# Optimization experiments

Hardware: AMD Instinct MI355X
Metric: run time of the kernel (lower is better)

## Reference

```python
import jax, jax.numpy as jnp
import numpy as np

E, H, D, F = 768, 12, 64, 3072
SCALE = D ** -0.5
EPS = 1e-5


def setup_inputs() -> dict:
    key = jax.random.key(0)
    ks = jax.random.split(key, 12)
    B, S = 8, 1024
    x = jax.random.normal(ks[0], (B, S, E), jnp.float32)
    # causal additive mask: 0 on/below diagonal, large negative above
    causal = jnp.triu(jnp.full((S, S), -1e9, jnp.float32), k=1)
    mask = jnp.broadcast_to(causal, (B, 1, S, S))
    init = lambda k, shp: jax.random.normal(k, shp, jnp.float32) * (shp[0] ** -0.5)
    return {
        "x": x, "mask": mask,
        "ln1_g": jnp.ones((E,), jnp.float32), "ln1_b": jnp.zeros((E,), jnp.float32),
        "wq": init(ks[1], (E, E)), "bq": jnp.zeros((E,), jnp.float32),
        "wk": init(ks[2], (E, E)), "bk": jnp.zeros((E,), jnp.float32),
        "wv": init(ks[3], (E, E)), "bv": jnp.zeros((E,), jnp.float32),
        "wo": init(ks[4], (E, E)), "bo": jnp.zeros((E,), jnp.float32),
        "ln2_g": jnp.ones((E,), jnp.float32), "ln2_b": jnp.zeros((E,), jnp.float32),
        "w1": init(ks[5], (E, F)), "b1": jnp.zeros((F,), jnp.float32),
        "w2": init(ks[6], (F, E)), "b2": jnp.zeros((E,), jnp.float32),
    }


def _layernorm(x, g, b):
    mu = jnp.mean(x, axis=-1, keepdims=True)
    var = jnp.var(x, axis=-1, keepdims=True)
    return (x - mu) * jax.lax.rsqrt(var + EPS) * g + b


def _attention(h, mask, wq, bq, wk, bk, wv, bv, wo, bo):
    B, S, _ = h.shape
    split = lambda t: t.reshape(B, S, H, D).transpose(0, 2, 1, 3)  # (B,H,S,D)
    q = split((h @ wq + bq) * SCALE)
    k = split(h @ wk + bk)
    v = split(h @ wv + bv)
    scores = jnp.einsum("bhqd,bhkd->bhqk", q, k) + mask
    attn = jax.nn.softmax(scores, axis=-1)
    o = jnp.einsum("bhqk,bhkd->bhqd", attn, v)
    o = o.transpose(0, 2, 1, 3).reshape(B, S, E)
    return o @ wo + bo


def reference(x, mask, ln1_g, ln1_b, wq, bq, wk, bk, wv, bv, wo, bo,
              ln2_g, ln2_b, w1, b1, w2, b2):
    h = _layernorm(x, ln1_g, ln1_b)
    h = x + _attention(h, mask, wq, bq, wk, bk, wv, bv, wo, bo)
    m = _layernorm(h, ln2_g, ln2_b)
    m = jax.nn.gelu(m @ w1 + b1, approximate=False) @ w2 + b2
    return h + m
```

## Files before the change

### kernel.cpp

```cpp
#include <hip/hip_runtime.h>
#include <hip/hip_bf16.h>

#define E_ 768
#define H_ 12
#define D_ 64
#define F_ 3072
#define S_ 1024
#define B_ 8
#define R_ 8192

typedef __attribute__((ext_vector_type(4))) float f32x4;
typedef __attribute__((ext_vector_type(8))) short bf16x8;

__device__ __forceinline__ short f2bf(float f) {
  unsigned u = __builtin_bit_cast(unsigned, f);
  u = (u + 0x7FFFu + ((u >> 16) & 1u)) >> 16;
  return (short)u;
}

__device__ __forceinline__ f32x4 mfma16(bf16x8 a, bf16x8 b, f32x4 c) {
  return __builtin_amdgcn_mfma_f32_16x16x32_bf16(a, b, c, 0, 0, 0);
}

#define GLD_LDS(g, l) __builtin_amdgcn_global_load_lds( \
    (const __attribute__((address_space(1))) void*)(g), \
    (__attribute__((address_space(3))) void*)(l), 16, 0, 0)

__global__ __launch_bounds__(256) void transpose_cast_kernel(
    const float* __restrict__ src, short* __restrict__ dst, int K, int N, float scale) {
  __shared__ float t[32][33];
  int k0 = blockIdx.x * 32, n0 = blockIdx.y * 32;
  int tr = threadIdx.x >> 5, tc = threadIdx.x & 31;
#pragma unroll
  for (int i = 0; i < 4; i++) {
    int r = i * 8 + tr;
    t[r][tc] = src[(long)(k0 + r) * N + n0 + tc] * scale;
  }
  __syncthreads();
#pragma unroll
  for (int i = 0; i < 4; i++) {
    int r = i * 8 + tr;
    dst[(long)(n0 + r) * K + k0 + tc] = f2bf(t[tc][r]);
  }
}

__global__ __launch_bounds__(256) void biasprep_kernel(
    const float* __restrict__ bq, const float* __restrict__ bk,
    const float* __restrict__ bv, float* __restrict__ dst) {
  int i = blockIdx.x * 256 + threadIdx.x;
  const float QS = 0.125f * 1.44269504088896340736f;
  if (i < 2304) {
    dst[i] = i < 768 ? QS * bq[i] : (i < 1536 ? bk[i - 768] : bv[i - 1536]);
  }
}

__global__ __launch_bounds__(256) void ln_kernel(
    const float* __restrict__ in, const float* __restrict__ g,
    const float* __restrict__ bb, short* __restrict__ outp) {
  int w = threadIdx.x >> 6, l = threadIdx.x & 63;
  long row = (long)blockIdx.x * 4 + w;
  const float4* r4 = (const float4*)(in + row * E_);
  float4 v[3];
  float s = 0.f, ss = 0.f;
#pragma unroll
  for (int i = 0; i < 3; i++) {
    v[i] = r4[i * 64 + l];
    s += v[i].x + v[i].y + v[i].z + v[i].w;
    ss += v[i].x * v[i].x + v[i].y * v[i].y + v[i].z * v[i].z + v[i].w * v[i].w;
  }
#pragma unroll
  for (int m = 1; m < 64; m <<= 1) { s += __shfl_xor(s, m); ss += __shfl_xor(ss, m); }
  float mu = s * (1.f / E_);
  float inv = rsqrtf(ss * (1.f / E_) - mu * mu + 1e-5f);
  const float4* g4 = (const float4*)g;
  const float4* b4 = (const float4*)bb;
  short4* o4 = (short4*)(outp + row * E_);
#pragma unroll
  for (int i = 0; i < 3; i++) {
    float4 gg = g4[i * 64 + l], bv = b4[i * 64 + l];
    short4 o;
    o.x = f2bf((v[i].x - mu) * inv * gg.x + bv.x);
    o.y = f2bf((v[i].y - mu) * inv * gg.y + bv.y);
    o.z = f2bf((v[i].z - mu) * inv * gg.z + bv.z);
    o.w = f2bf((v[i].w - mu) * inv * gg.w + bv.w);
    o4[i * 64 + l] = o;
  }
}

__global__ __launch_bounds__(256) void transpose_v_kernel(
    const short* __restrict__ v, short* __restrict__ vt) {
  __shared__ short t[64][68];
  int sb = blockIdx.x, p = blockIdx.y;
  const short* src = v + ((long)p * S_ + sb * 64) * 64;
  int tid = threadIdx.x;
#pragma unroll
  for (int i = 0; i < 4; i++) {
    int lin = tid + i * 256;
    int s = lin >> 4, c4 = lin & 15;
    short4 val = *(const short4*)(src + s * 64 + c4 * 4);
    t[s][c4 * 4 + 0] = val.x; t[s][c4 * 4 + 1] = val.y;
    t[s][c4 * 4 + 2] = val.z; t[s][c4 * 4 + 3] = val.w;
  }
  __syncthreads();
#pragma unroll
  for (int i = 0; i < 4; i++) {
    int lin = tid + i * 256;
    int d = lin >> 4, c4 = lin & 15;
    short4 o;
    o.x = t[c4 * 4 + 0][d]; o.y = t[c4 * 4 + 1][d];
    o.z = t[c4 * 4 + 2][d]; o.w = t[c4 * 4 + 3][d];
    *(short4*)(vt + ((long)p * 64 + d) * S_ + sb * 64 + c4 * 4) = o;
  }
}

template <int EPI>
__global__ __launch_bounds__(256) void gemm_bt(
    const short* __restrict__ A, const short* __restrict__ BT,
    const float* __restrict__ bias, const float* __restrict__ res,
    void* __restrict__ o0, void* __restrict__ o1, void* __restrict__ o2,
    int M, int N, int K) {
  __shared__ short lA[128 * 32];
  __shared__ short lB[128 * 32];
  int tid = threadIdx.x;
  int bm = blockIdx.x, bn = blockIdx.y;
  int w = tid >> 6, l = tid & 63;
  int wr = w >> 1, wc = w & 1;
  int lr = l & 15, lg = l >> 4;

  const f32x4 fz = {0.f, 0.f, 0.f, 0.f};
  f32x4 acc[4][4];
#pragma unroll
  for (int i = 0; i < 4; i++)
#pragma unroll
    for (int j = 0; j < 4; j++) acc[i][j] = fz;

  const short* Ab = A + (long)bm * 128 * K;
  const short* Bb = BT + (long)bn * 128 * K;
  int r0 = tid >> 2, kk0 = (tid & 3) * 8;
  int wb = (tid & 192) * 8;

  for (int k0 = 0; k0 < K; k0 += 32) {
    const short* ga0 = Ab + (long)r0 * K + k0 + kk0;
    const short* gb0 = Bb + (long)r0 * K + k0 + kk0;
    GLD_LDS(ga0, lA + wb);
    GLD_LDS(ga0 + (long)64 * K, lA + 2048 + wb);
    GLD_LDS(gb0, lB + wb);
    GLD_LDS(gb0 + (long)64 * K, lB + 2048 + wb);
    __syncthreads();
    bf16x8 af[4], bf[4];
#pragma unroll
    for (int m = 0; m < 4; m++) af[m] = *(const bf16x8*)&lA[(wr * 64 + m * 16 + lr) * 32 + lg * 8];
#pragma unroll
    for (int n = 0; n < 4; n++) bf[n] = *(const bf16x8*)&lB[(wc * 64 + n * 16 + lr) * 32 + lg * 8];
#pragma unroll
    for (int m = 0; m < 4; m++)
#pragma unroll
      for (int n = 0; n < 4; n++) acc[m][n] = mfma16(af[m], bf[n], acc[m][n]);
    __syncthreads();
  }

  int rb = bm * 128 + wr * 64;
  int cb = bn * 128 + wc * 64;
  if constexpr (EPI == 0) {
    int part = (bn * 128) / 768;
    short* dst = part == 0 ? (short*)o0 : (part == 1 ? (short*)o1 : (short*)o2);
#pragma unroll
    for (int m = 0; m < 4; m++)
#pragma unroll
      for (int n = 0; n < 4; n++) {
        int col = cb + n * 16 + lr;
        int e = col - part * 768;
        int hh = e >> 6, d = e & 63;
        float bc = bias[col];
#pragma unroll
        for (int r = 0; r < 4; r++) {
          int row = rb + m * 16 + lg * 4 + r;
          int bbi = row >> 10, sI = row & 1023;
          dst[((long)(bbi * H_ + hh) * S_ + sI) * D_ + d] = f2bf(acc[m][n][r] + bc);
        }
      }
  } else if constexpr (EPI == 1) {
    float* o = (float*)o0;
#pragma unroll
    for (int m = 0; m < 4; m++)
#pragma unroll
      for (int n = 0; n < 4; n++) {
        int col = cb + n * 16 + lr;
        float bc = bias[col];
#pragma unroll
        for (int r = 0; r < 4; r++) {
          long idx = (long)(rb + m * 16 + lg * 4 + r) * N + col;
          o[idx] = acc[m][n][r] + bc + res[idx];
        }
      }
  } else {
    short* o = (short*)o0;
#pragma unroll
    for (int m = 0; m < 4; m++)
#pragma unroll
      for (int n = 0; n < 4; n++) {
        int col = cb + n * 16 + lr;
        float bc = bias[col];
#pragma unroll
        for (int r = 0; r < 4; r++) {
          long idx = (long)(rb + m * 16 + lg * 4 + r) * N + col;
          float vv = acc[m][n][r] + bc;
          vv = 0.5f * vv * (1.f + erff(vv * 0.70710678118654752f));
          o[idx] = f2bf(vv);
        }
      }
  }
}

__global__ __launch_bounds__(256) void attn_kernel(
    const short* __restrict__ Qg, const short* __restrict__ Kg,
    const short* __restrict__ VT, short* __restrict__ Og) {
  __shared__ unsigned pl[2][4][16][36];
  int tid = threadIdx.x;
  int w = tid >> 6, l = tid & 63;
  int lr = l & 15, lg = l >> 4;
  int i = blockIdx.x;
  int qa0 = i * 64;
  int qb0 = (15 - i) * 64;
  int ph = blockIdx.y;
  int b = ph / H_, h = ph - b * H_;
  const short* Q = Qg + (long)ph * S_ * D_;
  const short* Kp = Kg + (long)ph * S_ * D_;
  const short* Vt = VT + (long)ph * D_ * S_;

  int qrA = qa0 + w * 16 + lr;
  int qrB = qb0 + w * 16 + lr;
  bf16x8 qfA0 = *(const bf16x8*)&Q[(long)qrA * 64 + lg * 8];
  bf16x8 qfA1 = *(const bf16x8*)&Q[(long)qrA * 64 + 32 + lg * 8];
  bf16x8 qfB0 = *(const bf16x8*)&Q[(long)qrB * 64 + lg * 8];
  bf16x8 qfB1 = *(const bf16x8*)&Q[(long)qrB * 64 + 32 + lg * 8];

  const f32x4 fz = {0.f, 0.f, 0.f, 0.f};
  f32x4 oaccA[4], oaccB[4];
#pragma unroll
  for (int n = 0; n < 4; n++) { oaccA[n] = fz; oaccB[n] = fz; }
  float mA = -__builtin_inff(), lA = 0.f;
  float mB = -__builtin_inff(), lB = 0.f;

  for (int k0 = 0; k0 <= qb0; k0 += 64) {
    bool doA = (k0 <= qa0);
    bf16x8 kf[4][2], vf[4][2];
#pragma unroll
    for (int n = 0; n < 4; n++) {
      kf[n][0] = *(const bf16x8*)&Kp[(long)(k0 + n * 16 + lr) * 64 + lg * 8];
      kf[n][1] = *(const bf16x8*)&Kp[(long)(k0 + n * 16 + lr) * 64 + 32 + lg * 8];
      vf[n][0] = *(const bf16x8*)&Vt[(long)(n * 16 + lr) * S_ + k0 + lg * 8];
      vf[n][1] = *(const bf16x8*)&Vt[(long)(n * 16 + lr) * S_ + k0 + 32 + lg * 8];
    }
    f32x4 scB[4], scA[4];
#pragma unroll
    for (int n = 0; n < 4; n++) {
      scB[n] = mfma16(kf[n][0], qfB0, fz);
      scB[n] = mfma16(kf[n][1], qfB1, scB[n]);
    }
    if (doA) {
#pragma unroll
      for (int n = 0; n < 4; n++) {
        scA[n] = mfma16(kf[n][0], qfA0, fz);
        scA[n] = mfma16(kf[n][1], qfA1, scA[n]);
      }
    }
    if (k0 == qb0) {
#pragma unroll
      for (int n = 0; n < 4; n++)
#pragma unroll
        for (int r = 0; r < 4; r++)
          if (n * 16 + lg * 4 + r > w * 16 + lr) scB[n][r] = -1e30f;
    }
    if (doA && k0 == qa0) {
#pragma unroll
      for (int n = 0; n < 4; n++)
#pragma unroll
        for (int r = 0; r < 4; r++)
          if (n * 16 + lg * 4 + r > w * 16 + lr) scA[n][r] = -1e30f;
    }
    float tB = scB[0][0];
#pragma unroll
    for (int n = 0; n < 4; n++)
#pragma unroll
      for (int r = 0; r < 4; r++) tB = fmaxf(tB, scB[n][r]);
    tB = fmaxf(tB, __shfl_xor(tB, 16));
    tB = fmaxf(tB, __shfl_xor(tB, 32));
    float mnB = fmaxf(mB, tB);
    float corrB = exp2f(mB - mnB);
    float psB = 0.f;
#pragma unroll
    for (int n = 0; n < 4; n++)
#pragma unroll
      for (int r = 0; r < 4; r++) {
        float p = exp2f(scB[n][r] - mnB);
        scB[n][r] = p;
        psB += p;
      }
    psB += __shfl_xor(psB, 16);
    psB += __shfl_xor(psB, 32);
    lB = lB * corrB + psB;
    mB = mnB;
    float corrA = 1.f;
    if (doA) {
      float tA = scA[0][0];
#pragma unroll
      for (int n = 0; n < 4; n++)
#pragma unroll
        for (int r = 0; r < 4; r++) tA = fmaxf(tA, scA[n][r]);
      tA = fmaxf(tA, __shfl_xor(tA, 16));
      tA = fmaxf(tA, __shfl_xor(tA, 32));
      float mnA = fmaxf(mA, tA);
      corrA = exp2f(mA - mnA);
      float psA = 0.f;
#pragma unroll
      for (int n = 0; n < 4; n++)
#pragma unroll
        for (int r = 0; r < 4; r++) {
          float p = exp2f(scA[n][r] - mnA);
          scA[n][r] = p;
          psA += p;
        }
      psA += __shfl_xor(psA, 16);
      psA += __shfl_xor(psA, 32);
      lA = lA * corrA + psA;
      mA = mnA;
    }
#pragma unroll
    for (int n = 0; n < 4; n++) {
      uint2 pr;
      pr.x = (unsigned)(unsigned short)f2bf(scB[n][0]) |
             ((unsigned)(unsigned short)f2bf(scB[n][1]) << 16);
      pr.y = (unsigned)(unsigned short)f2bf(scB[n][2]) |
             ((unsigned)(unsigned short)f2bf(scB[n][3]) << 16);
      *(uint2*)&pl[1][w][lr][n * 8 + lg * 2] = pr;
    }
    if (doA) {
#pragma unroll
      for (int n = 0; n < 4; n++) {
        uint2 pr;
        pr.x = (unsigned)(unsigned short)f2bf(scA[n][0]) |
               ((unsigned)(unsigned short)f2bf(scA[n][1]) << 16);
        pr.y = (unsigned)(unsigned short)f2bf(scA[n][2]) |
               ((unsigned)(unsigned short)f2bf(scA[n][3]) << 16);
        *(uint2*)&pl[0][w][lr][n * 8 + lg * 2] = pr;
      }
    }
    bf16x8 pbB0 = *(const bf16x8*)&pl[1][w][lr][lg * 4];
    bf16x8 pbB1 = *(const bf16x8*)&pl[1][w][lr][16 + lg * 4];
#pragma unroll
    for (int n = 0; n < 4; n++) {
#pragma unroll
      for (int r = 0; r < 4; r++) oaccB[n][r] *= corrB;
      oaccB[n] = mfma16(vf[n][0], pbB0, oaccB[n]);
      oaccB[n] = mfma16(vf[n][1], pbB1, oaccB[n]);
    }
    if (doA) {
      bf16x8 pbA0 = *(const bf16x8*)&pl[0][w][lr][lg * 4];
      bf16x8 pbA1 = *(const bf16x8*)&pl[0][w][lr][16 + lg * 4];
#pragma unroll
      for (int n = 0; n < 4; n++) {
#pragma unroll
        for (int r = 0; r < 4; r++) oaccA[n][r] *= corrA;
        oaccA[n] = mfma16(vf[n][0], pbA0, oaccA[n]);
        oaccA[n] = mfma16(vf[n][1], pbA1, oaccA[n]);
      }
    }
  }

  float invA = 1.f / lA, invB = 1.f / lB;
  long obA = ((long)b * S_ + qrA) * E_ + h * D_;
  long obB = ((long)b * S_ + qrB) * E_ + h * D_;
#pragma unroll
  for (int n = 0; n < 4; n++) {
    short4 oa, ob;
    oa.x = f2bf(oaccA[n][0] * invA); oa.y = f2bf(oaccA[n][1] * invA);
    oa.z = f2bf(oaccA[n][2] * invA); oa.w = f2bf(oaccA[n][3] * invA);
    ob.x = f2bf(oaccB[n][0] * invB); ob.y = f2bf(oaccB[n][1] * invB);
    ob.z = f2bf(oaccB[n][2] * invB); ob.w = f2bf(oaccB[n][3] * invB);
    *(short4*)&Og[obA + n * 16 + lg * 4] = oa;
    *(short4*)&Og[obB + n * 16 + lg * 4] = ob;
  }
}

extern "C" void kernel_launch(void* const* d_in, const int* in_sizes, int n_in,
                              void* d_out, int out_size, void* d_ws, size_t ws_size,
                              hipStream_t stream) {
  (void)in_sizes; (void)n_in; (void)out_size; (void)ws_size;
  const float* x    = (const float*)d_in[0];
  const float* ln1g = (const float*)d_in[2];
  const float* ln1b = (const float*)d_in[3];
  const float* wq   = (const float*)d_in[4];
  const float* bq   = (const float*)d_in[5];
  const float* wk   = (const float*)d_in[6];
  const float* bk   = (const float*)d_in[7];
  const float* wv   = (const float*)d_in[8];
  const float* bv   = (const float*)d_in[9];
  const float* wo   = (const float*)d_in[10];
  const float* bo   = (const float*)d_in[11];
  const float* ln2g = (const float*)d_in[12];
  const float* ln2b = (const float*)d_in[13];
  const float* w1   = (const float*)d_in[14];
  const float* b1   = (const float*)d_in[15];
  const float* w2   = (const float*)d_in[16];
  const float* b2   = (const float*)d_in[17];
  float* out = (float*)d_out;
  char* ws = (char*)d_ws;

  constexpr size_t SZ_WQKVT = (size_t)2304 * 768 * 2;
  constexpr size_t SZ_WOT   = (size_t)768 * 768 * 2;
  constexpr size_t SZ_W1T   = (size_t)3072 * 768 * 2;
  constexpr size_t SZ_W2T   = (size_t)768 * 3072 * 2;
  constexpr size_t SZ_BQKV  = (size_t)2304 * 4;
  constexpr size_t SZ_H1    = (size_t)R_ * 768 * 2;
  constexpr size_t SZ_HB    = (size_t)R_ * 768 * 4;
  constexpr size_t SZ_QKV1  = (size_t)R_ * 768 * 2;

  size_t off = 0;
  short* WQKVT = (short*)(ws + off); off += SZ_WQKVT;
  short* WOT   = (short*)(ws + off); off += SZ_WOT;
  short* W1T   = (short*)(ws + off); off += SZ_W1T;
  short* W2T   = (short*)(ws + off); off += SZ_W2T;
  float* BQKV  = (float*)(ws + off); off += SZ_BQKV;
  short* H1    = (short*)(ws + off); off += SZ_H1;
  float* HB    = (float*)(ws + off); off += SZ_HB;
  size_t qoff = off;
  short* Qb    = (short*)(ws + off); off += SZ_QKV1;
  short* Kb    = (short*)(ws + off); off += SZ_QKV1;
  short* Vb    = (short*)(ws + off); off += SZ_QKV1;
  short* VTb   = (short*)(ws + off); off += SZ_QKV1;
  short* Ob    = Vb;
  short* Abuf  = (short*)(ws + qoff);

  dim3 blk(256);
  const float QS = 0.125f * 1.44269504088896340736f;
  transpose_cast_kernel<<<dim3(24, 24), blk, 0, stream>>>(wq, WQKVT, 768, 768, QS);
  transpose_cast_kernel<<<dim3(24, 24), blk, 0, stream>>>(wk, WQKVT + 768 * 768, 768, 768, 1.f);
  transpose_cast_kernel<<<dim3(24, 24), blk, 0, stream>>>(wv, WQKVT + 2 * 768 * 768, 768, 768, 1.f);
  transpose_cast_kernel<<<dim3(24, 24), blk, 0, stream>>>(wo, WOT, 768, 768, 1.f);
  transpose_cast_kernel<<<dim3(24, 96), blk, 0, stream>>>(w1, W1T, 768, 3072, 1.f);
  transpose_cast_kernel<<<dim3(96, 24), blk, 0, stream>>>(w2, W2T, 3072, 768, 1.f);
  biasprep_kernel<<<9, blk, 0, stream>>>(bq, bk, bv, BQKV);

  ln_kernel<<<R_ / 4, blk, 0, stream>>>(x, ln1g, ln1b, H1);
  gemm_bt<0><<<dim3(64, 18), blk, 0, stream>>>(H1, WQKVT, BQKV, nullptr, Qb, Kb, Vb, R_, 2304, 768);
  transpose_v_kernel<<<dim3(16, 96), blk, 0, stream>>>(Vb, VTb);
  attn_kernel<<<dim3(8, 96), blk, 0, stream>>>(Qb, Kb, VTb, Ob);
  gemm_bt<1><<<dim3(64, 6), blk, 0, stream>>>(Ob, WOT, bo, x, HB, nullptr, nullptr, R_, 768, 768);
  ln_kernel<<<R_ / 4, blk, 0, stream>>>(HB, ln2g, ln2b, H1);
  gemm_bt<2><<<dim3(64, 24), blk, 0, stream>>>(H1, W1T, b1, nullptr, Abuf, nullptr, nullptr, R_, 3072, 768);
  gemm_bt<1><<<dim3(64, 6), blk, 0, stream>>>(Abuf, W2T, b2, HB, out, nullptr, nullptr, R_, 768, 3072);
}
```

Baseline: 492.4 us.

## Prefetch next K/V tile in registers and swap attention grid dimensions

The attention loop now loads the next 64-key K and V^T fragments into registers while the current tile's score MFMAs and softmax run, then rotates them in at the end of the iteration. This software pipelining hides global-load latency, at the cost of roughly doubling the K/V fragment registers, which may lower occupancy. The launch grid is also transposed so that consecutive blocks cover different heads/batches for the same query-pair index, which changes block scheduling order and the balance of causal work.

```diff
diff --git a/kernel.cpp b/kernel.cpp
--- a/kernel.cpp
+++ b/kernel.cpp
@@ -219,10 +219,10 @@
   int tid = threadIdx.x;
   int w = tid >> 6, l = tid & 63;
   int lr = l & 15, lg = l >> 4;
-  int i = blockIdx.x;
+  int ph = blockIdx.x;
+  int i = blockIdx.y;
   int qa0 = i * 64;
   int qb0 = (15 - i) * 64;
-  int ph = blockIdx.y;
   int b = ph / H_, h = ph - b * H_;
   const short* Q = Qg + (long)ph * S_ * D_;
   const short* Kp = Kg + (long)ph * S_ * D_;
@@ -242,16 +242,19 @@
   float mA = -__builtin_inff(), lA = 0.f;
   float mB = -__builtin_inff(), lB = 0.f;
 
+  bf16x8 kf[4][2], vf[4][2];
+#pragma unroll
+  for (int n = 0; n < 4; n++) {
+    kf[n][0] = *(const bf16x8*)&Kp[(long)(n * 16 + lr) * 64 + lg * 8];
+    kf[n][1] = *(const bf16x8*)&Kp[(long)(n * 16 + lr) * 64 + 32 + lg * 8];
+    vf[n][0] = *(const bf16x8*)&Vt[(long)(n * 16 + lr) * S_ + lg * 8];
+    vf[n][1] = *(const bf16x8*)&Vt[(long)(n * 16 + lr) * S_ + 32 + lg * 8];
+  }
+
   for (int k0 = 0; k0 <= qb0; k0 += 64) {
     bool doA = (k0 <= qa0);
-    bf16x8 kf[4][2], vf[4][2];
-#pragma unroll
-    for (int n = 0; n < 4; n++) {
-      kf[n][0] = *(const bf16x8*)&Kp[(long)(k0 + n * 16 + lr) * 64 + lg * 8];
-      kf[n][1] = *(const bf16x8*)&Kp[(long)(k0 + n * 16 + lr) * 64 + 32 + lg * 8];
-      vf[n][0] = *(const bf16x8*)&Vt[(long)(n * 16 + lr) * S_ + k0 + lg * 8];
-      vf[n][1] = *(const bf16x8*)&Vt[(long)(n * 16 + lr) * S_ + k0 + 32 + lg * 8];
-    }
+    bool pf = (k0 + 64 <= qb0);
+
     f32x4 scB[4], scA[4];
 #pragma unroll
     for (int n = 0; n < 4; n++) {
@@ -263,6 +266,17 @@
       for (int n = 0; n < 4; n++) {
         scA[n] = mfma16(kf[n][0], qfA0, fz);
         scA[n] = mfma16(kf[n][1], qfA1, scA[n]);
+      }
+    }
+    bf16x8 kn[4][2], vn[4][2];
+    if (pf) {
+      int kB = k0 + 64;
+#pragma unroll
+      for (int n = 0; n < 4; n++) {
+        kn[n][0] = *(const bf16x8*)&Kp[(long)(kB + n * 16 + lr) * 64 + lg * 8];
+        kn[n][1] = *(const bf16x8*)&Kp[(long)(kB + n * 16 + lr) * 64 + 32 + lg * 8];
+        vn[n][0] = *(const bf16x8*)&Vt[(long)(n * 16 + lr) * S_ + kB + lg * 8];
+        vn[n][1] = *(const bf16x8*)&Vt[(long)(n * 16 + lr) * S_ + kB + 32 + lg * 8];
       }
     }
     if (k0 == qb0) {
@@ -364,6 +378,13 @@
         for (int r = 0; r < 4; r++) oaccA[n][r] *= corrA;
         oaccA[n] = mfma16(vf[n][0], pbA0, oaccA[n]);
         oaccA[n] = mfma16(vf[n][1], pbA1, oaccA[n]);
+      }
+    }
+    if (pf) {
+#pragma unroll
+      for (int n = 0; n < 4; n++) {
+        kf[n][0] = kn[n][0]; kf[n][1] = kn[n][1];
+        vf[n][0] = vn[n][0]; vf[n][1] = vn[n][1];
       }
     }
   }
@@ -445,7 +466,7 @@
   ln_kernel<<<R_ / 4, blk, 0, stream>>>(x, ln1g, ln1b, H1);
   gemm_bt<0><<<dim3(64, 18), blk, 0, stream>>>(H1, WQKVT, BQKV, nullptr, Qb, Kb, Vb, R_, 2304, 768);
   transpose_v_kernel<<<dim3(16, 96), blk, 0, stream>>>(Vb, VTb);
-  attn_kernel<<<dim3(8, 96), blk, 0, stream>>>(Qb, Kb, VTb, Ob);
+  attn_kernel<<<dim3(96, 8), blk, 0, stream>>>(Qb, Kb, VTb, Ob);
   gemm_bt<1><<<dim3(64, 6), blk, 0, stream>>>(Ob, WOT, bo, x, HB, nullptr, nullptr, R_, 768, 768);
   ln_kernel<<<R_ / 4, blk, 0, stream>>>(HB, ln2g, ln2b, H1);
   gemm_bt<2><<<dim3(64, 24), blk, 0, stream>>>(H1, W1T, b1, nullptr, Abuf, nullptr, nullptr, R_, 3072, 768);
```

Measured after the change: 480.5 us. 1.02x faster.
